# Optimization experiments

Measured on AMD Instinct MI355X. Metric: run time of the kernel, lower is better.

Reference implementation:

```python
import jax, jax.numpy as jnp
import numpy as np

OUT_X = OUT_Y = OUT_Z = 12        # out_size
N_VOX = OUT_X * OUT_Y * OUT_Z
N_ROIS, N_PTS, C = 128, 160000, 64


def setup_inputs() -> dict:
    key = jax.random.key(0)
    k1, k2, k3, k4, k5, k6 = jax.random.split(key, 6)
    # rois: (N, 7) = [x, y, z_bottom, w(dx), l(dy), h(dz), ry]
    centers_xy = jax.random.uniform(k1, (N_ROIS, 2), minval=-40.0, maxval=40.0)
    z_bottom = jax.random.uniform(k2, (N_ROIS, 1), minval=-2.0, maxval=0.0)
    sizes = jax.random.uniform(k3, (N_ROIS, 3), minval=1.5, maxval=5.0)
    ry = jax.random.uniform(k4, (N_ROIS, 1), minval=-np.pi, maxval=np.pi)
    rois = jnp.concatenate([centers_xy, z_bottom, sizes, ry], axis=1).astype(jnp.float32)
    # points spread over the same scene extent so many fall inside rois
    pts = (jax.random.uniform(k5, (N_PTS, 3), minval=-1.0, maxval=1.0)
           * jnp.array([45.0, 45.0, 2.5], jnp.float32)).astype(jnp.float32)
    pts_feature = jax.random.normal(k6, (N_PTS, C), dtype=jnp.float32)
    return {"rois": rois, "pts": pts, "pts_feature": pts_feature}


def _voxel_segments(rois, pts):
    """Per (roi, point): flat voxel index in [0, N_VOX), or N_VOX if outside the roi."""
    cx, cy, cz, dx, dy, dz, rz = [rois[:, i:i + 1] for i in range(7)]  # (N,1)
    sx = pts[:, 0] - cx   # (N,P)
    sy = pts[:, 1] - cy
    sz = pts[:, 2] - cz   # z relative to box bottom
    cosa, sina = jnp.cos(-rz), jnp.sin(-rz)
    lx = sx * cosa - sy * sina  # rotate into roi-local frame
    ly = sx * sina + sy * cosa
    in_box = ((lx > -dx * 0.5) & (lx < dx * 0.5)
              & (ly > -dy * 0.5) & (ly < dy * 0.5)
              & (jnp.abs(sz - dz * 0.5) <= dz * 0.5))
    xi = jnp.clip(jnp.floor((lx + dx * 0.5) / (dx / OUT_X)), 0, OUT_X - 1).astype(jnp.int32)
    yi = jnp.clip(jnp.floor((ly + dy * 0.5) / (dy / OUT_Y)), 0, OUT_Y - 1).astype(jnp.int32)
    zi = jnp.clip(jnp.floor(sz / (dz / OUT_Z)), 0, OUT_Z - 1).astype(jnp.int32)
    seg = xi * (OUT_Y * OUT_Z) + yi * OUT_Z + zi
    return jnp.where(in_box, seg, N_VOX)  # (N, P) int32


def reference(rois, pts, pts_feature):
    seg = _voxel_segments(rois, pts)  # (N, P)
    ones = jnp.ones((pts.shape[0],), jnp.float32)

    def per_roi(s):
        mx = jax.ops.segment_max(pts_feature, s, num_segments=N_VOX + 1)[:N_VOX]  # (V, C)
        cnt = jax.ops.segment_sum(ones, s, num_segments=N_VOX + 1)[:N_VOX]        # (V,)
        return jnp.where(cnt[:, None] > 0, mx, 0.0)  # empty voxels -> 0, as in CUDA kernel

    pooled = jax.lax.map(per_roi, seg)  # (N, V, C); sequential over rois keeps memory bounded
    return pooled.reshape(N_ROIS, OUT_X, OUT_Y, OUT_Z, pts_feature.shape[-1])
```

## Files before the change

kernel.cpp:

```cpp
#include <hip/hip_runtime.h>

#define NROIS 128
#define OUTD  12
#define NVOX  (OUTD * OUTD * OUTD)
#define NCH   64
#define NKEYS (NROIS * NVOX)
#define RPB   16
#define QCAP  1024
#define STAMP 0x5AFE5AFEu

__device__ __forceinline__ unsigned enc_f32(float f) {
    unsigned b = __float_as_uint(f);
    return (b & 0x80000000u) ? ~b : (b | 0x80000000u);
}

__device__ __forceinline__ float dec_key(unsigned k) {
    unsigned b = (k & 0x80000000u) ? (k & 0x7fffffffu) : ~k;
    return __uint_as_float(b);
}

__global__ void __launch_bounds__(256) roi_pool_scatter(
        const float* __restrict__ rois,
        const float* __restrict__ pts,
        const float* __restrict__ feat,
        unsigned*    __restrict__ out,
        unsigned*    __restrict__ stamp,
        int npts)
{
    __shared__ float4   sRej[RPB];
    __shared__ float    sRad[RPB];
    __shared__ float4   sFull[RPB * 3];
    __shared__ unsigned sQp[QCAP];
    __shared__ unsigned sQk[QCAP];
    __shared__ unsigned sQn;

    int rbase = blockIdx.y * RPB;
    if (threadIdx.x == 0) sQn = 0;
    if (threadIdx.x < RPB) {
        int r = rbase + threadIdx.x;
        float cx = rois[7 * r + 0];
        float cy = rois[7 * r + 1];
        float cz = rois[7 * r + 2];
        float dx = rois[7 * r + 3];
        float dy = rois[7 * r + 4];
        float dz = rois[7 * r + 5];
        float nrz = -rois[7 * r + 6];
        float ca = cosf(nrz), sa = sinf(nrz);
        float hx = __fmul_rn(dx, 0.5f);
        float hy = __fmul_rn(dy, 0.5f);
        float hz = __fmul_rn(dz, 0.5f);
        sFull[3 * threadIdx.x + 0] = make_float4(cx, cy, cz, ca);
        sFull[3 * threadIdx.x + 1] = make_float4(sa, hx, hy, hz);
        sFull[3 * threadIdx.x + 2] = make_float4(__fdiv_rn(dx, 12.0f),
                                                 __fdiv_rn(dy, 12.0f),
                                                 __fdiv_rn(dz, 12.0f), 0.0f);
        float R2 = 0.25f * (dx * dx + dy * dy);
        sRad[threadIdx.x] = R2 * 1.04f + 1e-4f;
        sRej[threadIdx.x] = make_float4(cx, cy, cz + hz, hz * 1.001f + 1e-3f);
    }
    __syncthreads();

    int p = blockIdx.x * blockDim.x + threadIdx.x;
    if (p < npts) {
        float px = pts[3 * p + 0];
        float py = pts[3 * p + 1];
        float pz = pts[3 * p + 2];

        unsigned hm = 0;
        #pragma unroll
        for (int r = 0; r < RPB; ++r) {
            float4 q = sRej[r];
            float sx = px - q.x;
            float sy = py - q.y;
            float d2 = sx * sx + sy * sy;
            bool maybe = (d2 < sRad[r]) & (fabsf(pz - q.z) <= q.w);
            hm |= ((unsigned)maybe) << r;
        }

        while (hm) {
            int r = __ffs(hm) - 1;
            hm &= hm - 1;
            float4 F0 = sFull[3 * r + 0];
            float4 F1 = sFull[3 * r + 1];
            float sx = __fsub_rn(px, F0.x);
            float sy = __fsub_rn(py, F0.y);
            float sz = __fsub_rn(pz, F0.z);
            float ca = F0.w, sa = F1.x;
            float hx = F1.y, hy = F1.z, hz = F1.w;
            float lx = __fsub_rn(__fmul_rn(sx, ca), __fmul_rn(sy, sa));
            float ly = __fadd_rn(__fmul_rn(sx, sa), __fmul_rn(sy, ca));

            bool in_box = (lx > -hx) && (lx < hx) &&
                          (ly > -hy) && (ly < hy) &&
                          (fabsf(__fsub_rn(sz, hz)) <= hz);
            if (!in_box) continue;

            float4 F2 = sFull[3 * r + 2];
            int xi = (int)floorf(__fdiv_rn(__fadd_rn(lx, hx), F2.x));
            int yi = (int)floorf(__fdiv_rn(__fadd_rn(ly, hy), F2.y));
            int zi = (int)floorf(__fdiv_rn(sz,                F2.z));
            xi = min(max(xi, 0), OUTD - 1);
            yi = min(max(yi, 0), OUTD - 1);
            zi = min(max(zi, 0), OUTD - 1);

            unsigned key = (unsigned)((rbase + r) * NVOX +
                                      xi * (OUTD * OUTD) + yi * OUTD + zi);

            unsigned idx = atomicAdd(&sQn, 1u);
            if (idx < QCAP) {
                sQp[idx] = (unsigned)p;
                sQk[idx] = key;
            } else {
                stamp[key] = STAMP;
                unsigned* dst = out + (size_t)key * NCH;
                const float* fp = feat + (size_t)p * NCH;
                #pragma unroll 1
                for (int c = 0; c < NCH; ++c)
                    atomicMax(dst + c, enc_f32(fp[c]));
            }
        }
    }

    __syncthreads();
    int nq   = min((int)sQn, QCAP);
    int wid  = threadIdx.x >> 6;
    int lane = threadIdx.x & 63;
    for (int i = wid; i < nq; i += 4) {
        unsigned pp = sQp[i];
        unsigned kk = sQk[i];
        if (lane == 0) stamp[kk] = STAMP;
        float f = feat[(size_t)pp * NCH + lane];
        atomicMax(out + (size_t)kk * NCH + lane, enc_f32(f));
    }
}

__global__ void __launch_bounds__(256) decode_touched(
        unsigned* __restrict__ out,
        const unsigned* __restrict__ stamp)
{
    int w    = (blockIdx.x * blockDim.x + threadIdx.x) >> 6;
    int lane = threadIdx.x & 63;
    int base = w * 64;
    if (base >= NKEYS) return;
    unsigned s = stamp[base + lane];
    unsigned long long m = __ballot(s == STAMP);
    while (m) {
        int b = __ffsll((long long)m) - 1;
        m &= m - 1;
        unsigned key = (unsigned)(base + b);
        unsigned* v = out + (size_t)key * NCH;
        unsigned k = v[lane];
        v[lane] = (k == 0u) ? 0u : __float_as_uint(dec_key(k));
    }
}

extern "C" void kernel_launch(void* const* d_in, const int* in_sizes, int n_in,
                              void* d_out, int out_size, void* d_ws, size_t ws_size,
                              hipStream_t stream)
{
    const float* rois = (const float*)d_in[0];
    const float* pts  = (const float*)d_in[1];
    const float* feat = (const float*)d_in[2];
    int npts = in_sizes[1] / 3;

    unsigned* stamp = (unsigned*)d_ws;

    hipMemsetAsync(d_out, 0, (size_t)out_size * sizeof(float), stream);

    dim3 grid((npts + 255) / 256, NROIS / RPB);
    roi_pool_scatter<<<grid, 256, 0, stream>>>(rois, pts, feat,
                                               (unsigned*)d_out, stamp, npts);

    decode_touched<<<NKEYS / 256, 256, 0, stream>>>((unsigned*)d_out, stamp);
}
```

Baseline: 115.7 us.

## Bin ROIs into a 2D grid to cull candidate ROIs per point

Adds a prep kernel that precomputes per-ROI parameters and builds an 18x18 spatial grid listing which ROIs overlap each cell, and that also zeroes the output in place of the memset. The scatter kernel now launches one block per 256 points covering all ROIs, testing only the ROIs in the point's cell rather than 16 ROIs per block across 8 grid rows. This removes the repeated point loads and the redundant rejection tests across ROI groups. Queue overflow now spills to a global buffer, replacing the per-channel atomic fallback. The cost is more queue pressure per block and per-point divergent loops over global ROI data.

```diff
diff --git a/kernel.cpp b/kernel.cpp
--- a/kernel.cpp
+++ b/kernel.cpp
@@ -5,9 +5,12 @@
 #define NVOX  (OUTD * OUTD * OUTD)
 #define NCH   64
 #define NKEYS (NROIS * NVOX)
-#define RPB   16
-#define QCAP  1024
+#define QCAP  2048
+#define OVF   2048
 #define STAMP 0x5AFE5AFEu
+#define CELLS 18
+#define NCELL (CELLS * CELLS)
+#define CSLOT 32
 
 __device__ __forceinline__ unsigned enc_f32(float f) {
     unsigned b = __float_as_uint(f);
@@ -19,69 +22,110 @@
     return __uint_as_float(b);
 }
 
+__global__ void __launch_bounds__(256) fill_prep(
+        const float* __restrict__ rois,
+        unsigned*    __restrict__ out,
+        float4*      __restrict__ prej,
+        float*       __restrict__ prad,
+        float4*      __restrict__ pfull,
+        int*         __restrict__ ccnt,
+        unsigned char* __restrict__ ctab)
+{
+    const int tid = threadIdx.x;
+    if (blockIdx.x == 0) {
+        __shared__ int           lcnt[NCELL];
+        __shared__ unsigned char ltab[NCELL * CSLOT];
+        for (int i = tid; i < NCELL; i += 256) lcnt[i] = 0;
+        __syncthreads();
+        if (tid < NROIS) {
+            int r = tid;
+            float cx = rois[7 * r + 0];
+            float cy = rois[7 * r + 1];
+            float cz = rois[7 * r + 2];
+            float dx = rois[7 * r + 3];
+            float dy = rois[7 * r + 4];
+            float dz = rois[7 * r + 5];
+            float nrz = -rois[7 * r + 6];
+            float ca = cosf(nrz), sa = sinf(nrz);
+            float hx = __fmul_rn(dx, 0.5f);
+            float hy = __fmul_rn(dy, 0.5f);
+            float hz = __fmul_rn(dz, 0.5f);
+            pfull[3 * r + 0] = make_float4(cx, cy, cz, ca);
+            pfull[3 * r + 1] = make_float4(sa, hx, hy, hz);
+            pfull[3 * r + 2] = make_float4(__fdiv_rn(dx, 12.0f),
+                                           __fdiv_rn(dy, 12.0f),
+                                           __fdiv_rn(dz, 12.0f), 0.0f);
+            float R2  = 0.25f * (dx * dx + dy * dy);
+            float R2m = R2 * 1.04f + 1e-4f;
+            prad[r] = R2m;
+            prej[r] = make_float4(cx, cy, cz + hz, hz * 1.001f + 1e-3f);
+            float rb = sqrtf(R2m) * 1.001f + 0.02f;
+            int x0 = min(max((int)floorf((cx - rb + 45.0f) * 0.2f), 0), CELLS - 1);
+            int x1 = min(max((int)floorf((cx + rb + 45.0f) * 0.2f), 0), CELLS - 1);
+            int y0 = min(max((int)floorf((cy - rb + 45.0f) * 0.2f), 0), CELLS - 1);
+            int y1 = min(max((int)floorf((cy + rb + 45.0f) * 0.2f), 0), CELLS - 1);
+            for (int xx = x0; xx <= x1; ++xx)
+                for (int yy = y0; yy <= y1; ++yy) {
+                    int c = xx * CELLS + yy;
+                    int s = atomicAdd(&lcnt[c], 1);
+                    if (s < CSLOT) ltab[c * CSLOT + s] = (unsigned char)r;
+                }
+        }
+        __syncthreads();
+        for (int i = tid; i < NCELL; i += 256) ccnt[i] = lcnt[i];
+        for (int i = tid; i < NCELL * CSLOT; i += 256) ctab[i] = ltab[i];
+    }
+    uint4* o16 = (uint4*)out;
+    const int tot16 = NKEYS * (NCH / 4);
+    const uint4 z = make_uint4(0u, 0u, 0u, 0u);
+    for (int i = blockIdx.x * 256 + tid; i < tot16; i += gridDim.x * 256)
+        o16[i] = z;
+}
+
 __global__ void __launch_bounds__(256) roi_pool_scatter(
-        const float* __restrict__ rois,
         const float* __restrict__ pts,
         const float* __restrict__ feat,
         unsigned*    __restrict__ out,
         unsigned*    __restrict__ stamp,
+        const float4* __restrict__ prej,
+        const float*  __restrict__ prad,
+        const float4* __restrict__ pfull,
+        const int*    __restrict__ ccnt,
+        const unsigned char* __restrict__ ctab,
+        unsigned long long*  __restrict__ ovf,
         int npts)
 {
-    __shared__ float4   sRej[RPB];
-    __shared__ float    sRad[RPB];
-    __shared__ float4   sFull[RPB * 3];
     __shared__ unsigned sQp[QCAP];
     __shared__ unsigned sQk[QCAP];
     __shared__ unsigned sQn;
 
-    int rbase = blockIdx.y * RPB;
-    if (threadIdx.x == 0) sQn = 0;
-    if (threadIdx.x < RPB) {
-        int r = rbase + threadIdx.x;
-        float cx = rois[7 * r + 0];
-        float cy = rois[7 * r + 1];
-        float cz = rois[7 * r + 2];
-        float dx = rois[7 * r + 3];
-        float dy = rois[7 * r + 4];
-        float dz = rois[7 * r + 5];
-        float nrz = -rois[7 * r + 6];
-        float ca = cosf(nrz), sa = sinf(nrz);
-        float hx = __fmul_rn(dx, 0.5f);
-        float hy = __fmul_rn(dy, 0.5f);
-        float hz = __fmul_rn(dz, 0.5f);
-        sFull[3 * threadIdx.x + 0] = make_float4(cx, cy, cz, ca);
-        sFull[3 * threadIdx.x + 1] = make_float4(sa, hx, hy, hz);
-        sFull[3 * threadIdx.x + 2] = make_float4(__fdiv_rn(dx, 12.0f),
-                                                 __fdiv_rn(dy, 12.0f),
-                                                 __fdiv_rn(dz, 12.0f), 0.0f);
-        float R2 = 0.25f * (dx * dx + dy * dy);
-        sRad[threadIdx.x] = R2 * 1.04f + 1e-4f;
-        sRej[threadIdx.x] = make_float4(cx, cy, cz + hz, hz * 1.001f + 1e-3f);
-    }
+    const int tid = threadIdx.x;
+    if (tid == 0) sQn = 0;
     __syncthreads();
 
-    int p = blockIdx.x * blockDim.x + threadIdx.x;
+    int p = blockIdx.x * 256 + tid;
     if (p < npts) {
         float px = pts[3 * p + 0];
         float py = pts[3 * p + 1];
         float pz = pts[3 * p + 2];
 
-        unsigned hm = 0;
-        #pragma unroll
-        for (int r = 0; r < RPB; ++r) {
-            float4 q = sRej[r];
-            float sx = px - q.x;
-            float sy = py - q.y;
-            float d2 = sx * sx + sy * sy;
-            bool maybe = (d2 < sRad[r]) & (fabsf(pz - q.z) <= q.w);
-            hm |= ((unsigned)maybe) << r;
-        }
-
-        while (hm) {
-            int r = __ffs(hm) - 1;
-            hm &= hm - 1;
-            float4 F0 = sFull[3 * r + 0];
-            float4 F1 = sFull[3 * r + 1];
+        int cxi  = min(max((int)floorf((px + 45.0f) * 0.2f), 0), CELLS - 1);
+        int cyi  = min(max((int)floorf((py + 45.0f) * 0.2f), 0), CELLS - 1);
+        int cell = cxi * CELLS + cyi;
+        int n    = ccnt[cell];
+        bool fallback = (n > CSLOT);
+        int  m = fallback ? NROIS : n;
+
+        for (int i = 0; i < m; ++i) {
+            int r = fallback ? i : (int)ctab[cell * CSLOT + i];
+            float4 q = prej[r];
+            float sx0 = px - q.x;
+            float sy0 = py - q.y;
+            float d2 = sx0 * sx0 + sy0 * sy0;
+            if (!((d2 < prad[r]) & (fabsf(pz - q.z) <= q.w))) continue;
+
+            float4 F0 = pfull[3 * r + 0];
+            float4 F1 = pfull[3 * r + 1];
             float sx = __fsub_rn(px, F0.x);
             float sy = __fsub_rn(py, F0.y);
             float sz = __fsub_rn(pz, F0.z);
@@ -95,7 +139,7 @@
                           (fabsf(__fsub_rn(sz, hz)) <= hz);
             if (!in_box) continue;
 
-            float4 F2 = sFull[3 * r + 2];
+            float4 F2 = pfull[3 * r + 2];
             int xi = (int)floorf(__fdiv_rn(__fadd_rn(lx, hx), F2.x));
             int yi = (int)floorf(__fdiv_rn(__fadd_rn(ly, hy), F2.y));
             int zi = (int)floorf(__fdiv_rn(sz,                F2.z));
@@ -103,31 +147,34 @@
             yi = min(max(yi, 0), OUTD - 1);
             zi = min(max(zi, 0), OUTD - 1);
 
-            unsigned key = (unsigned)((rbase + r) * NVOX +
+            unsigned key = (unsigned)(r * NVOX +
                                       xi * (OUTD * OUTD) + yi * OUTD + zi);
 
             unsigned idx = atomicAdd(&sQn, 1u);
             if (idx < QCAP) {
                 sQp[idx] = (unsigned)p;
                 sQk[idx] = key;
-            } else {
-                stamp[key] = STAMP;
-                unsigned* dst = out + (size_t)key * NCH;
-                const float* fp = feat + (size_t)p * NCH;
-                #pragma unroll 1
-                for (int c = 0; c < NCH; ++c)
-                    atomicMax(dst + c, enc_f32(fp[c]));
+            } else if (idx - QCAP < OVF) {
+                ovf[(size_t)blockIdx.x * OVF + (idx - QCAP)] =
+                    ((unsigned long long)key << 32) | (unsigned)p;
             }
         }
     }
 
     __syncthreads();
-    int nq   = min((int)sQn, QCAP);
-    int wid  = threadIdx.x >> 6;
-    int lane = threadIdx.x & 63;
+    int nq   = min((int)sQn, QCAP + OVF);
+    int wid  = tid >> 6;
+    int lane = tid & 63;
     for (int i = wid; i < nq; i += 4) {
-        unsigned pp = sQp[i];
-        unsigned kk = sQk[i];
+        unsigned pp, kk;
+        if (i < QCAP) {
+            pp = sQp[i];
+            kk = sQk[i];
+        } else {
+            unsigned long long e = ovf[(size_t)blockIdx.x * OVF + (i - QCAP)];
+            pp = (unsigned)e;
+            kk = (unsigned)(e >> 32);
+        }
         if (lane == 0) stamp[kk] = STAMP;
         float f = feat[(size_t)pp * NCH + lane];
         atomicMax(out + (size_t)kk * NCH + lane, enc_f32(f));
@@ -163,13 +210,22 @@
     const float* feat = (const float*)d_in[2];
     int npts = in_sizes[1] / 3;
 
-    unsigned* stamp = (unsigned*)d_ws;
-
-    hipMemsetAsync(d_out, 0, (size_t)out_size * sizeof(float), stream);
-
-    dim3 grid((npts + 255) / 256, NROIS / RPB);
-    roi_pool_scatter<<<grid, 256, 0, stream>>>(rois, pts, feat,
-                                               (unsigned*)d_out, stamp, npts);
-
-    decode_touched<<<NKEYS / 256, 256, 0, stream>>>((unsigned*)d_out, stamp);
-}
+    char* ws = (char*)d_ws;
+    unsigned*           stamp = (unsigned*)ws;
+    float4*             prej  = (float4*)(ws + (1 << 20));
+    float*              prad  = (float*) (ws + (1 << 20) + 2048);
+    float4*             pfull = (float4*)(ws + (1 << 20) + 4096);
+    int*                ccnt  = (int*)   (ws + (1 << 20) + 12288);
+    unsigned char*      ctab  = (unsigned char*)(ws + (1 << 20) + 16384);
+    unsigned long long* ovf   = (unsigned long long*)(ws + (2 << 20));
+    unsigned*           out   = (unsigned*)d_out;
+
+    fill_prep<<<2048, 256, 0, stream>>>(rois, out, prej, prad, pfull, ccnt, ctab);
+
+    int nblk = (npts + 255) / 256;
+    roi_pool_scatter<<<nblk, 256, 0, stream>>>(pts, feat, out, stamp,
+                                               prej, prad, pfull, ccnt, ctab,
+                                               ovf, npts);
+
+    decode_touched<<<NKEYS / 256, 256, 0, stream>>>(out, stamp);
+}
```

Result: no change. 115.9 us (+0.2%).
